# Kernel optimization log

Measured on AMD Instinct MI355X. Metric: run time of the kernel, lower is better.

Reference implementation:

```python
import jax, jax.numpy as jnp
import numpy as np

K = 2  # top-k routing (init kwarg k=2)


def setup_inputs() -> dict:
    key = jax.random.key(0)
    k1, k2 = jax.random.split(key)
    in_flow = jax.random.normal(k1, (8192, 2048), dtype=jnp.float32)
    gates = jax.random.uniform(k2, (8192, 8), dtype=jnp.float32)
    return {"in_flow": in_flow, "gates": gates}


def reference(in_flow, gates):
    # in_flow: [N, D] tokens; gates: [N, E]
    N, E = gates.shape
    # --- gen_indices (topk branch): one-hot-k routing mask [N, E] ---
    top_idx = jax.lax.top_k(gates, K)[1]                       # [N, K]
    mask = jnp.zeros((N, E), dtype=jnp.int32)
    mask = mask.at[jnp.arange(N)[:, None], top_idx].set(1)     # scatter_(1, idx, 1)
    # --- dispatch: per-expert gather, concatenated expert-major ---
    # torch.nonzero(mask.T[i]) returns token indices ascending per expert;
    # stable argsort of expert-major flattened mask reproduces exactly that
    # concatenation order, and topk guarantees exactly N*K selected rows.
    flat = mask.T.reshape(-1)                                  # [E*N], expert-major
    order = jnp.argsort(-flat)                                 # stable: ones first, in order
    sel = order[: N * K]                                       # flat positions of assignments
    token_idx = sel % N                                        # [N*K] source token per row
    out_data = in_flow[token_idx]                              # [N*K, D] routed flow
    out_tags = token_idx                                       # tags (pack_invalid_flow arange tags)
    counts = mask.sum(axis=0)                                  # [E] rows per destination (loads)
    return out_data, out_tags, counts
```

## Files before the change

kernel.cpp:

```cpp
#include <hip/hip_runtime.h>
#include <hip/hip_bf16.h>


#define EXPERTS 8
#define TOPK 2
#define BLK 256

__global__ void k_mask_count(const float* __restrict__ gates,
                             int* __restrict__ masks,
                             int* __restrict__ block_counts) {
    int n = blockIdx.x * BLK + threadIdx.x;
    const float4* g4 = (const float4*)(gates + (size_t)n * EXPERTS);
    float4 a = g4[0], b = g4[1];
    float v[EXPERTS] = {a.x, a.y, a.z, a.w, b.x, b.y, b.z, b.w};

    int e1 = 0; float b1 = v[0];
    #pragma unroll
    for (int e = 1; e < EXPERTS; e++) if (v[e] > b1) { b1 = v[e]; e1 = e; }
    int e2 = -1; float b2 = -1e30f;
    #pragma unroll
    for (int e = 0; e < EXPERTS; e++) if (e != e1 && v[e] > b2) { b2 = v[e]; e2 = e; }

    int mask = (1 << e1) | (1 << e2);
    masks[n] = mask;

    int wave = threadIdx.x >> 6;
    int lane = threadIdx.x & 63;
    __shared__ int wc[BLK / 64][EXPERTS];
    #pragma unroll
    for (int e = 0; e < EXPERTS; e++) {
        unsigned long long bal = __ballot((mask >> e) & 1);
        if (lane == 0) wc[wave][e] = __popcll(bal);
    }
    __syncthreads();
    if (threadIdx.x < EXPERTS) {
        int e = threadIdx.x;
        int t = 0;
        #pragma unroll
        for (int w = 0; w < BLK / 64; w++) t += wc[w][e];
        block_counts[blockIdx.x * EXPERTS + e] = t;
    }
}

__global__ void k_scan(const int* __restrict__ block_counts,
                       int* __restrict__ block_offsets,
                       float* __restrict__ counts_out, int NB) {
    __shared__ int tot[EXPERTS];
    __shared__ int base[EXPERTS];
    int e = threadIdx.x;
    if (e < EXPERTS) {
        int t = 0;
        for (int b = 0; b < NB; b++) t += block_counts[b * EXPERTS + e];
        tot[e] = t;
        counts_out[e] = (float)t;
    }
    __syncthreads();
    if (threadIdx.x == 0) {
        int acc = 0;
        for (int i = 0; i < EXPERTS; i++) { base[i] = acc; acc += tot[i]; }
    }
    __syncthreads();
    if (e < EXPERTS) {
        int acc = base[e];
        for (int b = 0; b < NB; b++) {
            block_offsets[b * EXPERTS + e] = acc;
            acc += block_counts[b * EXPERTS + e];
        }
    }
}

__global__ void k_pos(const int* __restrict__ masks,
                      const int* __restrict__ block_offsets,
                      int* __restrict__ tok_of_pos) {
    int n = blockIdx.x * BLK + threadIdx.x;
    int mask = masks[n];
    int wave = threadIdx.x >> 6;
    int lane = threadIdx.x & 63;
    __shared__ int wc[BLK / 64][EXPERTS];
    unsigned long long bal[EXPERTS];
    #pragma unroll
    for (int e = 0; e < EXPERTS; e++) {
        bal[e] = __ballot((mask >> e) & 1);
        if (lane == 0) wc[wave][e] = __popcll(bal[e]);
    }
    __syncthreads();
    unsigned long long below = (lane == 0) ? 0ull : ((~0ull) >> (64 - lane));
    #pragma unroll
    for (int e = 0; e < EXPERTS; e++) {
        if ((mask >> e) & 1) {
            int wbase = 0;
            for (int w = 0; w < wave; w++) wbase += wc[w][e];
            int r = __popcll(bal[e] & below);
            int pos = block_offsets[blockIdx.x * EXPERTS + e] + wbase + r;
            tok_of_pos[pos] = n;
        }
    }
}

__global__ void k_copy(const float* __restrict__ in_flow,
                       const int* __restrict__ tok_of_pos,
                       float* __restrict__ out_data,
                       float* __restrict__ out_tags, int D) {
    int p = blockIdx.x;
    int tok = tok_of_pos[p];
    if (threadIdx.x == 0) out_tags[p] = (float)tok;
    const float4* src = (const float4*)(in_flow + (size_t)tok * D);
    float4* dst = (float4*)(out_data + (size_t)p * D);
    int nv = D >> 2;
    for (int i = threadIdx.x; i < nv; i += BLK) dst[i] = src[i];
}

extern "C" void kernel_launch(void* const* d_in, const int* in_sizes, int n_in,
                              void* d_out, int out_size, void* d_ws, size_t ws_size,
                              hipStream_t stream) {
    const float* in_flow = (const float*)d_in[0];
    const float* gates   = (const float*)d_in[1];

    const int N  = in_sizes[1] / EXPERTS;
    const int D  = in_sizes[0] / N;
    const int NB = (N + BLK - 1) / BLK;
    const int NK = N * TOPK;

    int* masks         = (int*)d_ws;
    int* block_counts  = masks + N;
    int* block_offsets = block_counts + NB * EXPERTS;
    int* tok_of_pos    = block_offsets + NB * EXPERTS;

    float* out_data  = (float*)d_out;
    float* out_tags  = out_data + (size_t)NK * D;
    float* counts_out = out_tags + NK;

    hipLaunchKernelGGL(k_mask_count, dim3(NB), dim3(BLK), 0, stream,
                       gates, masks, block_counts);
    hipLaunchKernelGGL(k_scan, dim3(1), dim3(64), 0, stream,
                       block_counts, block_offsets, counts_out, NB);
    hipLaunchKernelGGL(k_pos, dim3(NB), dim3(BLK), 0, stream,
                       masks, block_offsets, tok_of_pos);
    hipLaunchKernelGGL(k_copy, dim3(NK), dim3(BLK), 0, stream,
                       in_flow, tok_of_pos, out_data, out_tags, D);
}
```

Measured before the change: 197.7 us.

## Fuse routing into single-block scan kernel and scatter-copy each token once

Replaces the three routing kernels (mask+count, scan, position) with one 1024-thread single-block kernel. Each thread handles 8 tokens, packs per-expert counts into 16-bit lanes, and prefix-scans them with wave shuffles to produce each token's two destination positions. The copy kernel now runs per source token, reading each input row once and writing it to both destinations with nontemporal stores, which halves input reads. The cost is hardcoded assumptions: N must equal 8192 (1024 threads × 8) and per-expert counts must fit in 16 bits. The single-block routing stage is also serial.

```diff
diff --git a/kernel.cpp b/kernel.cpp
--- a/kernel.cpp
+++ b/kernel.cpp
@@ -1,113 +1,121 @@
 #include <hip/hip_runtime.h>
-#include <hip/hip_bf16.h>
 
 
 #define EXPERTS 8
 #define TOPK 2
 #define BLK 256
+#define RTHREADS 1024
+#define TPT 8
 
-__global__ void k_mask_count(const float* __restrict__ gates,
-                             int* __restrict__ masks,
-                             int* __restrict__ block_counts) {
-    int n = blockIdx.x * BLK + threadIdx.x;
-    const float4* g4 = (const float4*)(gates + (size_t)n * EXPERTS);
-    float4 a = g4[0], b = g4[1];
-    float v[EXPERTS] = {a.x, a.y, a.z, a.w, b.x, b.y, b.z, b.w};
+typedef float f32x4 __attribute__((ext_vector_type(4)));
 
-    int e1 = 0; float b1 = v[0];
+__global__ __launch_bounds__(RTHREADS, 1)
+void k_route(const float* __restrict__ gates,
+             int2* __restrict__ pos_pair,
+             float* __restrict__ counts_out) {
+    const int t    = threadIdx.x;
+    const int lane = t & 63;
+    const int wave = t >> 6;
+
+    __shared__ unsigned int wt[RTHREADS / 64][4];
+    __shared__ unsigned int wb[RTHREADS / 64][4];
+    __shared__ int base8[EXPERTS];
+    __shared__ unsigned short soff[RTHREADS][EXPERTS];
+
+    int epair[TPT];
+    unsigned long long cnt8 = 0ull;
+
     #pragma unroll
-    for (int e = 1; e < EXPERTS; e++) if (v[e] > b1) { b1 = v[e]; e1 = e; }
-    int e2 = -1; float b2 = -1e30f;
+    for (int j = 0; j < TPT; j++) {
+        const int n = t * TPT + j;
+        const float4* g4 = (const float4*)(gates + (size_t)n * EXPERTS);
+        float4 a = g4[0], b = g4[1];
+        float v[EXPERTS] = {a.x, a.y, a.z, a.w, b.x, b.y, b.z, b.w};
+        int e1 = 0; float b1 = v[0];
+        #pragma unroll
+        for (int e = 1; e < EXPERTS; e++) if (v[e] > b1) { b1 = v[e]; e1 = e; }
+        int e2 = -1; float b2 = -1e30f;
+        #pragma unroll
+        for (int e = 0; e < EXPERTS; e++) if (e != e1 && v[e] > b2) { b2 = v[e]; e2 = e; }
+        epair[j] = e1 | (e2 << 4);
+        cnt8 += (1ull << (e1 * 8)) + (1ull << (e2 * 8));
+    }
+
+    unsigned int lo = (unsigned int)cnt8, hi = (unsigned int)(cnt8 >> 32);
+    unsigned int c01 = (lo & 0xFFu)         | ((lo & 0xFF00u) << 8);
+    unsigned int c23 = ((lo >> 16) & 0xFFu) | ((lo >> 24) << 16);
+    unsigned int c45 = (hi & 0xFFu)         | ((hi & 0xFF00u) << 8);
+    unsigned int c67 = ((hi >> 16) & 0xFFu) | ((hi >> 24) << 16);
+
+    unsigned int s01 = c01, s23 = c23, s45 = c45, s67 = c67;
     #pragma unroll
-    for (int e = 0; e < EXPERTS; e++) if (e != e1 && v[e] > b2) { b2 = v[e]; e2 = e; }
+    for (int d = 1; d < 64; d <<= 1) {
+        unsigned int q01 = __shfl_up(s01, d), q23 = __shfl_up(s23, d);
+        unsigned int q45 = __shfl_up(s45, d), q67 = __shfl_up(s67, d);
+        if (lane >= d) { s01 += q01; s23 += q23; s45 += q45; s67 += q67; }
+    }
+    if (lane == 63) { wt[wave][0] = s01; wt[wave][1] = s23; wt[wave][2] = s45; wt[wave][3] = s67; }
+    __syncthreads();
 
-    int mask = (1 << e1) | (1 << e2);
-    masks[n] = mask;
-
-    int wave = threadIdx.x >> 6;
-    int lane = threadIdx.x & 63;
-    __shared__ int wc[BLK / 64][EXPERTS];
-    #pragma unroll
-    for (int e = 0; e < EXPERTS; e++) {
-        unsigned long long bal = __ballot((mask >> e) & 1);
-        if (lane == 0) wc[wave][e] = __popcll(bal);
+    if (t == 0) {
+        unsigned int a0 = 0, a1 = 0, a2 = 0, a3 = 0;
+        for (int w = 0; w < RTHREADS / 64; w++) {
+            wb[w][0] = a0; wb[w][1] = a1; wb[w][2] = a2; wb[w][3] = a3;
+            a0 += wt[w][0]; a1 += wt[w][1]; a2 += wt[w][2]; a3 += wt[w][3];
+        }
+        int tot[EXPERTS] = {(int)(a0 & 0xFFFF), (int)(a0 >> 16),
+                            (int)(a1 & 0xFFFF), (int)(a1 >> 16),
+                            (int)(a2 & 0xFFFF), (int)(a2 >> 16),
+                            (int)(a3 & 0xFFFF), (int)(a3 >> 16)};
+        int acc = 0;
+        for (int e = 0; e < EXPERTS; e++) {
+            base8[e] = acc; acc += tot[e];
+            counts_out[e] = (float)tot[e];
+        }
     }
     __syncthreads();
-    if (threadIdx.x < EXPERTS) {
-        int e = threadIdx.x;
-        int t = 0;
-        #pragma unroll
-        for (int w = 0; w < BLK / 64; w++) t += wc[w][e];
-        block_counts[blockIdx.x * EXPERTS + e] = t;
+
+    unsigned int x01 = wb[wave][0] + (s01 - c01);
+    unsigned int x23 = wb[wave][1] + (s23 - c23);
+    unsigned int x45 = wb[wave][2] + (s45 - c45);
+    unsigned int x67 = wb[wave][3] + (s67 - c67);
+    soff[t][0] = (unsigned short)(base8[0] + (x01 & 0xFFFF));
+    soff[t][1] = (unsigned short)(base8[1] + (x01 >> 16));
+    soff[t][2] = (unsigned short)(base8[2] + (x23 & 0xFFFF));
+    soff[t][3] = (unsigned short)(base8[3] + (x23 >> 16));
+    soff[t][4] = (unsigned short)(base8[4] + (x45 & 0xFFFF));
+    soff[t][5] = (unsigned short)(base8[5] + (x45 >> 16));
+    soff[t][6] = (unsigned short)(base8[6] + (x67 & 0xFFFF));
+    soff[t][7] = (unsigned short)(base8[7] + (x67 >> 16));
+
+    #pragma unroll
+    for (int j = 0; j < TPT; j++) {
+        const int n  = t * TPT + j;
+        const int e1 = epair[j] & 15, e2 = epair[j] >> 4;
+        const int p1 = soff[t][e1]++;
+        const int p2 = soff[t][e2]++;
+        pos_pair[n] = make_int2(p1, p2);
     }
 }
 
-__global__ void k_scan(const int* __restrict__ block_counts,
-                       int* __restrict__ block_offsets,
-                       float* __restrict__ counts_out, int NB) {
-    __shared__ int tot[EXPERTS];
-    __shared__ int base[EXPERTS];
-    int e = threadIdx.x;
-    if (e < EXPERTS) {
-        int t = 0;
-        for (int b = 0; b < NB; b++) t += block_counts[b * EXPERTS + e];
-        tot[e] = t;
-        counts_out[e] = (float)t;
+__global__ __launch_bounds__(BLK)
+void k_copy(const float* __restrict__ in_flow,
+            const int2* __restrict__ pos_pair,
+            float* __restrict__ out_data,
+            float* __restrict__ out_tags, int D) {
+    const int n = blockIdx.x;
+    const int2 pp = pos_pair[n];
+    if (threadIdx.x < 2) out_tags[threadIdx.x == 0 ? pp.x : pp.y] = (float)n;
+
+    const f32x4* __restrict__ src = (const f32x4*)(in_flow + (size_t)n * D);
+    f32x4* d0 = (f32x4*)(out_data + (size_t)pp.x * D);
+    f32x4* d1 = (f32x4*)(out_data + (size_t)pp.y * D);
+    const int nv = D >> 2;
+    for (int i = threadIdx.x; i < nv; i += BLK) {
+        f32x4 v = src[i];
+        __builtin_nontemporal_store(v, d0 + i);
+        __builtin_nontemporal_store(v, d1 + i);
     }
-    __syncthreads();
-    if (threadIdx.x == 0) {
-        int acc = 0;
-        for (int i = 0; i < EXPERTS; i++) { base[i] = acc; acc += tot[i]; }
-    }
-    __syncthreads();
-    if (e < EXPERTS) {
-        int acc = base[e];
-        for (int b = 0; b < NB; b++) {
-            block_offsets[b * EXPERTS + e] = acc;
-            acc += block_counts[b * EXPERTS + e];
-        }
-    }
-}
-
-__global__ void k_pos(const int* __restrict__ masks,
-                      const int* __restrict__ block_offsets,
-                      int* __restrict__ tok_of_pos) {
-    int n = blockIdx.x * BLK + threadIdx.x;
-    int mask = masks[n];
-    int wave = threadIdx.x >> 6;
-    int lane = threadIdx.x & 63;
-    __shared__ int wc[BLK / 64][EXPERTS];
-    unsigned long long bal[EXPERTS];
-    #pragma unroll
-    for (int e = 0; e < EXPERTS; e++) {
-        bal[e] = __ballot((mask >> e) & 1);
-        if (lane == 0) wc[wave][e] = __popcll(bal[e]);
-    }
-    __syncthreads();
-    unsigned long long below = (lane == 0) ? 0ull : ((~0ull) >> (64 - lane));
-    #pragma unroll
-    for (int e = 0; e < EXPERTS; e++) {
-        if ((mask >> e) & 1) {
-            int wbase = 0;
-            for (int w = 0; w < wave; w++) wbase += wc[w][e];
-            int r = __popcll(bal[e] & below);
-            int pos = block_offsets[blockIdx.x * EXPERTS + e] + wbase + r;
-            tok_of_pos[pos] = n;
-        }
-    }
-}
-
-__global__ void k_copy(const float* __restrict__ in_flow,
-                       const int* __restrict__ tok_of_pos,
-                       float* __restrict__ out_data,
-                       float* __restrict__ out_tags, int D) {
-    int p = blockIdx.x;
-    int tok = tok_of_pos[p];
-    if (threadIdx.x == 0) out_tags[p] = (float)tok;
-    const float4* src = (const float4*)(in_flow + (size_t)tok * D);
-    float4* dst = (float4*)(out_data + (size_t)p * D);
-    int nv = D >> 2;
-    for (int i = threadIdx.x; i < nv; i += BLK) dst[i] = src[i];
 }
 
 extern "C" void kernel_launch(void* const* d_in, const int* in_sizes, int n_in,
@@ -118,24 +126,16 @@
 
     const int N  = in_sizes[1] / EXPERTS;
     const int D  = in_sizes[0] / N;
-    const int NB = (N + BLK - 1) / BLK;
     const int NK = N * TOPK;
 
-    int* masks         = (int*)d_ws;
-    int* block_counts  = masks + N;
-    int* block_offsets = block_counts + NB * EXPERTS;
-    int* tok_of_pos    = block_offsets + NB * EXPERTS;
+    int2* pos_pair = (int2*)d_ws;
 
-    float* out_data  = (float*)d_out;
-    float* out_tags  = out_data + (size_t)NK * D;
+    float* out_data   = (float*)d_out;
+    float* out_tags   = out_data + (size_t)NK * D;
     float* counts_out = out_tags + NK;
 
-    hipLaunchKernelGGL(k_mask_count, dim3(NB), dim3(BLK), 0, stream,
-                       gates, masks, block_counts);
-    hipLaunchKernelGGL(k_scan, dim3(1), dim3(64), 0, stream,
-                       block_counts, block_offsets, counts_out, NB);
-    hipLaunchKernelGGL(k_pos, dim3(NB), dim3(BLK), 0, stream,
-                       masks, block_offsets, tok_of_pos);
-    hipLaunchKernelGGL(k_copy, dim3(NK), dim3(BLK), 0, stream,
-                       in_flow, tok_of_pos, out_data, out_tags, D);
+    hipLaunchKernelGGL(k_route, dim3(1), dim3(RTHREADS), 0, stream,
+                       gates, pos_pair, counts_out);
+    hipLaunchKernelGGL(k_copy, dim3(N), dim3(BLK), 0, stream,
+                       in_flow, pos_pair, out_data, out_tags, D);
 }
```

New measurement: 201.6 us. Within noise of the previous version (+2.0%).

## Fuse position computation into routing and copy each token once to both slots

Applied to the files above, without the earlier changes.

The routing kernel now computes each token's within-block rank for both selected experts and packs ranks and expert ids into one int, so the separate position kernel and the tok_of_pos buffer go away. The copy kernel is launched per source token instead of per output row. It reads each input row once with a nontemporal load and writes it to both destination rows, halving input reads and removing one launch. The packed format caps ranks at 9 bits, which assumes a block size of 256.

```diff
diff --git a/kernel.cpp b/kernel.cpp
--- a/kernel.cpp
+++ b/kernel.cpp
@@ -1,15 +1,21 @@
 #include <hip/hip_runtime.h>
-#include <hip/hip_bf16.h>
 
 
 #define EXPERTS 8
 #define TOPK 2
 #define BLK 256
 
-__global__ void k_mask_count(const float* __restrict__ gates,
-                             int* __restrict__ masks,
-                             int* __restrict__ block_counts) {
-    int n = blockIdx.x * BLK + threadIdx.x;
+typedef float f32x4 __attribute__((ext_vector_type(4)));
+
+__global__ __launch_bounds__(BLK)
+void k_route(const float* __restrict__ gates,
+             int* __restrict__ packed,
+             int* __restrict__ block_counts) {
+    const int tid  = threadIdx.x;
+    const int n    = blockIdx.x * BLK + tid;
+    const int lane = tid & 63;
+    const int wave = tid >> 6;
+
     const float4* g4 = (const float4*)(gates + (size_t)n * EXPERTS);
     float4 a = g4[0], b = g4[1];
     float v[EXPERTS] = {a.x, a.y, a.z, a.w, b.x, b.y, b.z, b.w};
@@ -21,24 +27,29 @@
     #pragma unroll
     for (int e = 0; e < EXPERTS; e++) if (e != e1 && v[e] > b2) { b2 = v[e]; e2 = e; }
 
-    int mask = (1 << e1) | (1 << e2);
-    masks[n] = mask;
+    const int mask = (1 << e1) | (1 << e2);
 
-    int wave = threadIdx.x >> 6;
-    int lane = threadIdx.x & 63;
     __shared__ int wc[BLK / 64][EXPERTS];
+    unsigned long long bal[EXPERTS];
     #pragma unroll
     for (int e = 0; e < EXPERTS; e++) {
-        unsigned long long bal = __ballot((mask >> e) & 1);
-        if (lane == 0) wc[wave][e] = __popcll(bal);
+        bal[e] = __ballot((mask >> e) & 1);
+        if (lane == 0) wc[wave][e] = __popcll(bal[e]);
     }
     __syncthreads();
-    if (threadIdx.x < EXPERTS) {
-        int e = threadIdx.x;
+
+    const unsigned long long below = (lane == 0) ? 0ull : ((~0ull) >> (64 - lane));
+    int r1 = __popcll(bal[e1] & below);
+    int r2 = __popcll(bal[e2] & below);
+    for (int w = 0; w < wave; w++) { r1 += wc[w][e1]; r2 += wc[w][e2]; }
+
+    packed[n] = r1 | (r2 << 9) | (e1 << 18) | (e2 << 21);
+
+    if (tid < EXPERTS) {
         int t = 0;
         #pragma unroll
-        for (int w = 0; w < BLK / 64; w++) t += wc[w][e];
-        block_counts[blockIdx.x * EXPERTS + e] = t;
+        for (int w = 0; w < BLK / 64; w++) t += wc[w][tid];
+        block_counts[blockIdx.x * EXPERTS + tid] = t;
     }
 }
 
@@ -69,45 +80,31 @@
     }
 }
 
-__global__ void k_pos(const int* __restrict__ masks,
-                      const int* __restrict__ block_offsets,
-                      int* __restrict__ tok_of_pos) {
-    int n = blockIdx.x * BLK + threadIdx.x;
-    int mask = masks[n];
-    int wave = threadIdx.x >> 6;
-    int lane = threadIdx.x & 63;
-    __shared__ int wc[BLK / 64][EXPERTS];
-    unsigned long long bal[EXPERTS];
-    #pragma unroll
-    for (int e = 0; e < EXPERTS; e++) {
-        bal[e] = __ballot((mask >> e) & 1);
-        if (lane == 0) wc[wave][e] = __popcll(bal[e]);
+__global__ __launch_bounds__(BLK)
+void k_copy(const float* __restrict__ in_flow,
+            const int* __restrict__ packed,
+            const int* __restrict__ block_offsets,
+            float* __restrict__ out_data,
+            float* __restrict__ out_tags, int D) {
+    const int n  = blockIdx.x;
+    const int pk = packed[n];
+    const int r1 = pk & 511, r2 = (pk >> 9) & 511;
+    const int e1 = (pk >> 18) & 7, e2 = (pk >> 21) & 7;
+    const int bo = (n >> 8) * EXPERTS;
+    const int p1 = block_offsets[bo + e1] + r1;
+    const int p2 = block_offsets[bo + e2] + r2;
+
+    if (threadIdx.x == 0) { out_tags[p1] = (float)n; out_tags[p2] = (float)n; }
+
+    const f32x4* __restrict__ src = (const f32x4*)(in_flow + (size_t)n * D);
+    f32x4* d0 = (f32x4*)(out_data + (size_t)p1 * D);
+    f32x4* d1 = (f32x4*)(out_data + (size_t)p2 * D);
+    const int nv = D >> 2;
+    for (int i = threadIdx.x; i < nv; i += BLK) {
+        f32x4 x = __builtin_nontemporal_load(src + i);
+        d0[i] = x;
+        d1[i] = x;
     }
-    __syncthreads();
-    unsigned long long below = (lane == 0) ? 0ull : ((~0ull) >> (64 - lane));
-    #pragma unroll
-    for (int e = 0; e < EXPERTS; e++) {
-        if ((mask >> e) & 1) {
-            int wbase = 0;
-            for (int w = 0; w < wave; w++) wbase += wc[w][e];
-            int r = __popcll(bal[e] & below);
-            int pos = block_offsets[blockIdx.x * EXPERTS + e] + wbase + r;
-            tok_of_pos[pos] = n;
-        }
-    }
-}
-
-__global__ void k_copy(const float* __restrict__ in_flow,
-                       const int* __restrict__ tok_of_pos,
-                       float* __restrict__ out_data,
-                       float* __restrict__ out_tags, int D) {
-    int p = blockIdx.x;
-    int tok = tok_of_pos[p];
-    if (threadIdx.x == 0) out_tags[p] = (float)tok;
-    const float4* src = (const float4*)(in_flow + (size_t)tok * D);
-    float4* dst = (float4*)(out_data + (size_t)p * D);
-    int nv = D >> 2;
-    for (int i = threadIdx.x; i < nv; i += BLK) dst[i] = src[i];
 }
 
 extern "C" void kernel_launch(void* const* d_in, const int* in_sizes, int n_in,
@@ -121,21 +118,18 @@
     const int NB = (N + BLK - 1) / BLK;
     const int NK = N * TOPK;
 
-    int* masks         = (int*)d_ws;
-    int* block_counts  = masks + N;
+    int* packed        = (int*)d_ws;
+    int* block_counts  = packed + N;
     int* block_offsets = block_counts + NB * EXPERTS;
-    int* tok_of_pos    = block_offsets + NB * EXPERTS;
 
-    float* out_data  = (float*)d_out;
-    float* out_tags  = out_data + (size_t)NK * D;
+    float* out_data   = (float*)d_out;
+    float* out_tags   = out_data + (size_t)NK * D;
     float* counts_out = out_tags + NK;
 
-    hipLaunchKernelGGL(k_mask_count, dim3(NB), dim3(BLK), 0, stream,
-                       gates, masks, block_counts);
+    hipLaunchKernelGGL(k_route, dim3(NB), dim3(BLK), 0, stream,
+                       gates, packed, block_counts);
     hipLaunchKernelGGL(k_scan, dim3(1), dim3(64), 0, stream,
                        block_counts, block_offsets, counts_out, NB);
-    hipLaunchKernelGGL(k_pos, dim3(NB), dim3(BLK), 0, stream,
-                       masks, block_offsets, tok_of_pos);
-    hipLaunchKernelGGL(k_copy, dim3(NK), dim3(BLK), 0, stream,
-                       in_flow, tok_of_pos, out_data, out_tags, D);
+    hipLaunchKernelGGL(k_copy, dim3(N), dim3(BLK), 0, stream,
+                       in_flow, packed, block_offsets, out_data, out_tags, D);
 }
```

Result: faster. 187.3 us (-5.2%).
